# Kernel tuning notes

Measured on AMD Instinct MI355X. Metric: run time of the kernel, lower is better.

Reference implementation:

```python
import jax, jax.numpy as jnp
import numpy as np

B_, T_, D_ = 4, 4096, 512
H_, DH_ = 8, 64
N_HASHES, BUCKET = 4, 64
SELF_ATTN_VAL = -5e4  # TOKEN_SELF_ATTN_VALUE from reformer-pytorch


def setup_inputs() -> dict:
    key = jax.random.key(0)
    ks = jax.random.split(key, 12)
    s = 0.02
    return {
        "src": jax.random.normal(ks[0], (B_, T_, D_), jnp.float32),
        "Wqk": jax.random.normal(ks[1], (D_, D_), jnp.float32) * s,
        "Wv": jax.random.normal(ks[2], (D_, D_), jnp.float32) * s,
        "Wout": jax.random.normal(ks[3], (D_, D_), jnp.float32) * s,
        "bout": jnp.zeros((D_,), jnp.float32),
        "W1": jax.random.normal(ks[4], (D_, 2048), jnp.float32) * s,
        "b1": jnp.zeros((2048,), jnp.float32),
        "W2": jax.random.normal(ks[5], (2048, D_), jnp.float32) * s,
        "b2": jnp.zeros((D_,), jnp.float32),
        "gamma": jnp.ones((D_,), jnp.float32),
        "beta": jnp.zeros((D_,), jnp.float32),
        "rotations": jax.random.normal(ks[6], (DH_, N_HASHES, (T_ // BUCKET) // 2), jnp.float32),
    }


def _look_one_back(x):
    # concat each chunk with the previous chunk (wraparound), along the slot axis
    prev = jnp.concatenate([x[:, -1:], x[:, :-1]], axis=1)
    return jnp.concatenate([x, prev], axis=2)


def lsh_attention(qk, v, rotations):
    # qk, v: (B, T, d) with B = batch*heads; shared-QK LSH attention (non-causal,
    # attend_across_buckets=True, allow_duplicate_attention=True, no dropout)
    B, T, d = qk.shape
    n_buckets = T // BUCKET
    # --- hashing ---
    rv = jnp.einsum("btf,fhi->bhti", qk, rotations)          # (B, n_hashes, T, nb/2)
    rv = jnp.concatenate([rv, -rv], axis=-1)                  # (B, n_hashes, T, nb)
    buckets = jnp.argmax(rv, axis=-1)                         # (B, n_hashes, T)
    offsets = (jnp.arange(N_HASHES) * n_buckets)[None, :, None]
    buckets = (buckets + offsets).reshape(B, N_HASHES * T)
    # --- sort by (bucket, position) ---
    ticker = jnp.arange(N_HASHES * T)
    buckets_and_t = buckets * T + (ticker % T)[None, :]
    sticker = jnp.argsort(buckets_and_t, axis=-1)             # (B, n_hashes*T)
    undo_sort = jnp.argsort(sticker, axis=-1)
    st = sticker % T
    sqk = jnp.take_along_axis(qk, st[..., None], axis=1)      # (B, n_hashes*T, d)
    sv = jnp.take_along_axis(v, st[..., None], axis=1)
    # --- chunk ---
    chunks = N_HASHES * n_buckets
    bq_t = st.reshape(B, chunks, BUCKET)
    bqk = sqk.reshape(B, chunks, BUCKET, d)
    bv = sv.reshape(B, chunks, BUCKET, d)
    bq = bqk
    bk = bqk / (jnp.linalg.norm(bqk, axis=-1, keepdims=True) + 1e-6)
    bk = _look_one_back(bk)                                   # (B, chunks, 2*BUCKET, d)
    bv = _look_one_back(bv)
    bkv_t = _look_one_back(bq_t)                              # (B, chunks, 2*BUCKET)
    # --- attention within chunk (+ one look-back chunk) ---
    dots = jnp.einsum("bcie,bcje->bcij", bq, bk) * (d ** -0.5)
    self_mask = bq_t[:, :, :, None] == bkv_t[:, :, None, :]
    dots = jnp.where(self_mask, SELF_ATTN_VAL, dots)
    lse = jax.nn.logsumexp(dots, axis=-1, keepdims=True)
    p = jnp.exp(dots - lse)
    bo = jnp.einsum("bcij,bcje->bcie", p, bv)
    # --- unsort and combine hash rounds ---
    so = bo.reshape(B, N_HASHES * T, d)
    slog = lse.reshape(B, N_HASHES * T)
    o = jnp.take_along_axis(so, undo_sort[..., None], axis=1)
    logits = jnp.take_along_axis(slog, undo_sort, axis=1)
    o = o.reshape(B, N_HASHES, T, d)
    logits = logits.reshape(B, N_HASHES, T, 1)
    probs = jnp.exp(logits - jax.nn.logsumexp(logits, axis=1, keepdims=True))
    return jnp.sum(o * probs, axis=1)                         # (B, T, d)


def _layer(src, Wqk, Wv, Wout, bout, W1, b1, W2, b2, gamma, beta, rotations):
    b, t, dm = src.shape
    qk = src @ Wqk
    v = src @ Wv
    def split(x):
        return x.reshape(b, t, H_, DH_).transpose(0, 2, 1, 3).reshape(b * H_, t, DH_)
    o = lsh_attention(split(qk), split(v), rotations)
    o = o.reshape(b, H_, t, DH_).transpose(0, 2, 1, 3).reshape(b, t, dm)
    attn_out = o @ Wout + bout
    x = src + attn_out                # residual (dropout = identity in eval)
    ffn = jax.nn.relu(x @ W1 + b1) @ W2 + b2
    y = x + ffn
    mu = jnp.mean(y, axis=-1, keepdims=True)
    var = jnp.mean((y - mu) ** 2, axis=-1, keepdims=True)
    return (y - mu) / jnp.sqrt(var + 1e-6) * gamma + beta     # post-norm (norm2)


def reference(src, Wqk, Wv, Wout, bout, W1, b1, W2, b2, gamma, beta, rotations):
    return _layer(src, Wqk, Wv, Wout, bout, W1, b1, W2, b2, gamma, beta, rotations)
```

## Files before the change

kernel.cpp:

```cpp
#include <hip/hip_runtime.h>

#define B_ 4
#define T_ 4096
#define D_ 512
#define H_ 8
#define DH_ 64
#define NH_ 4
#define NB_ 64
#define BH_ (B_*H_)
#define CHUNKS_ (NH_*NB_)
#define NTICK_ (NH_*T_)
#define M_ (B_*T_)
#define FFN_ 2048

typedef __attribute__((ext_vector_type(8))) short bf16x8;
typedef __attribute__((ext_vector_type(4))) float f32x4;

__device__ __forceinline__ unsigned short f2bf(float x) {
  unsigned int u = __float_as_uint(x);
  return (unsigned short)((u + 0x7FFFu + ((u >> 16) & 1u)) >> 16);
}
__device__ __forceinline__ float bf2f(unsigned short s) {
  return __uint_as_float(((unsigned int)s) << 16);
}
__device__ __forceinline__ unsigned int cvt_pk_bf16(float lo, float hi) {
  unsigned int r;
  asm("v_cvt_pk_bf16_f32 %0, %1, %2" : "=v"(r) : "v"(lo), "v"(hi));
  return r;
}

__device__ __forceinline__ void gld_lds16(const void* g, void* l) {
  __builtin_amdgcn_global_load_lds(
      (const __attribute__((address_space(1))) unsigned int*)g,
      (__attribute__((address_space(3))) unsigned int*)l, 16, 0, 0);
}

__device__ __forceinline__ int swf(int row) { return (row ^ (row >> 3)) & 7; }
__device__ __forceinline__ int off64(int row, int k) {
  return row * 64 + (((k >> 3) ^ swf(row)) << 3) + (k & 7);
}
__device__ __forceinline__ int off128(int row, int k) {
  return row * 128 + (((k >> 3) ^ swf(row)) << 3) + (k & 7);
}

template<int OM>
__global__ __launch_bounds__(512) void gemm256(
    const unsigned short* __restrict__ A, const unsigned short* __restrict__ BT,
    const float* __restrict__ bias, unsigned short* __restrict__ Cb,
    unsigned short* __restrict__ Cb2, float* __restrict__ Cf,
    float* __restrict__ invn, int M, int N, int K)
{
  constexpr int ABSZ = 32768;
  __shared__ __align__(16) unsigned short smem[2 * ABSZ];
  const int tid = threadIdx.x;
  const int lane = tid & 63, w = tid >> 6;
  const int wm = (w >> 2) * 128, wn = (w & 3) * 64;
  const int g = lane >> 4, cl = lane & 15;

  const int gx = gridDim.x;
  const int id = blockIdx.x + blockIdx.y * gx;
  const int cpx = (gx * gridDim.y) >> 3;
  const int swz = (id & 7) * cpx + (id >> 3);
  const int m0 = (swz / gx) * 256, n0 = (swz % gx) * 256;

  const bool isv = (OM == 1) && (n0 >= 512);

  f32x4 acc[8][4];
#pragma unroll
  for (int i = 0; i < 8; ++i)
#pragma unroll
    for (int j = 0; j < 4; ++j) acc[i][j] = (f32x4){0.f, 0.f, 0.f, 0.f};

#define STG256(BUF, KB, P)                                                    \
  do {                                                                        \
    const bool isA_ = (P) < 2;                                                \
    const int half_ = (P) & 1;                                                \
    const unsigned short* Mp_ = isA_ ? A : BT;                                \
    const int gb_ = isA_ ? m0 : n0;                                           \
    const int ro_ = isA_ ? 0 : 16384;                                         \
    _Pragma("unroll")                                                         \
    for (int c2 = 0; c2 < 2; ++c2) {                                          \
      const int r_ = half_ * 128 + w * 16 + c2 * 8 + (lane >> 3);             \
      const int kg_ = (lane & 7) ^ swf(r_);                                   \
      gld_lds16(&Mp_[(size_t)(gb_ + r_) * K + (KB) + kg_ * 8],                \
                &smem[(BUF) * ABSZ + ro_ +                                    \
                      (half_ * 128 + w * 16 + c2 * 8) * 64 + lane * 8]);      \
    }                                                                         \
  } while (0)

#pragma unroll
  for (int p = 0; p < 4; ++p) STG256(0, 0, p);

  const int KT = K >> 6;
  for (int kt = 0; kt < KT; ++kt) {
    const int cur = kt & 1;
    const unsigned short* As = smem + cur * ABSZ;
    const unsigned short* Bs = As + 16384;
#pragma unroll
    for (int p = 0; p < 4; ++p) {
      if (kt + 1 < KT) STG256(cur ^ 1, (kt + 1) * 64, p);
      if (p == 0) {
        if (kt + 1 < KT) asm volatile("s_waitcnt vmcnt(2)" ::: "memory");
        else             asm volatile("s_waitcnt vmcnt(0)" ::: "memory");
        __builtin_amdgcn_s_barrier();
      }
      const int rq = wm + (p >> 1) * 64, cq = wn + (p & 1) * 32;
      bf16x8 af[4][2], bfr[2][2];
#pragma unroll
      for (int i = 0; i < 4; ++i)
#pragma unroll
        for (int kk = 0; kk < 2; ++kk)
          af[i][kk] = *(const bf16x8*)&As[off64(rq + i * 16 + cl, kk * 32 + g * 8)];
#pragma unroll
      for (int j = 0; j < 2; ++j)
#pragma unroll
        for (int kk = 0; kk < 2; ++kk)
          bfr[j][kk] = *(const bf16x8*)&Bs[off64(cq + j * 16 + cl, kk * 32 + g * 8)];
      __builtin_amdgcn_s_setprio(1);
#pragma unroll
      for (int kk = 0; kk < 2; ++kk)
#pragma unroll
        for (int i = 0; i < 4; ++i)
#pragma unroll
          for (int j = 0; j < 2; ++j)
            acc[(p >> 1) * 4 + i][(p & 1) * 2 + j] =
                __builtin_amdgcn_mfma_f32_16x16x32_bf16(
                    af[i][kk], bfr[j][kk], acc[(p >> 1) * 4 + i][(p & 1) * 2 + j], 0, 0, 0);
      __builtin_amdgcn_s_setprio(0);
      if (p == 3) __builtin_amdgcn_s_barrier();
    }
  }
#undef STG256

  float bv[4];
  if constexpr (OM == 0) {
#pragma unroll
    for (int j4 = 0; j4 < 4; ++j4) bv[j4] = bias[n0 + wn + j4 * 16 + cl];
  }
#pragma unroll
  for (int i = 0; i < 8; ++i) {
#pragma unroll
    for (int r = 0; r < 4; ++r) {
      const int lrow = wm + i * 16 + g * 4 + r;
      const int sw = (lrow & 7) << 3;
      float v4[4];
      float ss = 0.f;
#pragma unroll
      for (int j4 = 0; j4 < 4; ++j4) {
        float val = acc[i][j4][r];
        if constexpr (OM == 0) val = fmaxf(val + bv[j4], 0.f);
        v4[j4] = val;
        if constexpr (OM == 1) {
          if (!isv) {
            ss += val * val;
            Cf[(size_t)(m0 + lrow) * 512 + n0 + wn + j4 * 16 + cl] = val;
          }
        }
      }
#pragma unroll
      for (int j4 = 0; j4 < 4; j4 += 2) {
        const unsigned int pk = cvt_pk_bf16(v4[j4], v4[j4 + 1]);
        smem[lrow * 256 + ((wn + j4 * 16 + cl) ^ sw)]       = (unsigned short)pk;
        smem[lrow * 256 + ((wn + (j4 + 1) * 16 + cl) ^ sw)] = (unsigned short)(pk >> 16);
      }
      if constexpr (OM == 1) {
        if (!isv) {
          ss += __shfl_xor(ss, 1); ss += __shfl_xor(ss, 2);
          ss += __shfl_xor(ss, 4); ss += __shfl_xor(ss, 8);
          if (cl == 0) {
            const int m = m0 + lrow;
            const int bb = m >> 12, t = m & (T_ - 1);
            const int hh = ((n0 + wn) >> 6) & 7;
            invn[((size_t)(bb * 8 + hh)) * T_ + t] = 1.0f / (sqrtf(ss) + 1e-6f);
          }
        }
      }
    }
  }
  __syncthreads();
#pragma unroll
  for (int l = 0; l < 16; ++l) {
    const int idx = tid + l * 512;
    const int row = idx >> 5, c8 = (idx & 31) * 8;
    const uint4 u = *(const uint4*)&smem[row * 256 + (c8 ^ ((row & 7) << 3))];
    if constexpr (OM == 1) {
      if (isv)
        *(uint4*)&Cb2[(size_t)(m0 + row) * 512 + (n0 - 512) + c8] = u;
      else
        *(uint4*)&Cb[(size_t)(m0 + row) * 512 + n0 + c8] = u;
    } else {
      *(uint4*)&Cb[(size_t)(m0 + row) * N + n0 + c8] = u;
    }
  }
}

template<int BM, int MODE, bool HAS_BIAS, bool RELU, bool HAS_RESID>
__global__ __launch_bounds__(256) void gemm_bf16(
    const unsigned short* __restrict__ A, const unsigned short* __restrict__ BT,
    const float* __restrict__ bias, const unsigned short* __restrict__ resid,
    float* __restrict__ Cf, unsigned short* __restrict__ Cb,
    unsigned short* __restrict__ Cb2, float* __restrict__ invn,
    int M, int N, int K, int lda, int ldbt, int ldr)
{
  constexpr int MI = BM / 32;
  constexpr int ABSZ = (BM + 128) * 64;
  __shared__ __align__(16) unsigned short smem[2 * ABSZ];
  const int tid = threadIdx.x;
  const int lane = tid & 63;
  const int w = tid >> 6;
  const int wm = (w >> 1) * (BM / 2), wn = (w & 1) * 64;
  const int g = lane >> 4, cl = lane & 15;

  const int gx = gridDim.x;
  const int id = blockIdx.x + blockIdx.y * gx;
  const int cpx = (gx * gridDim.y) >> 3;
  const int swz = (id & 7) * cpx + (id >> 3);
  const int m0 = (swz / gx) * BM, n0 = (swz % gx) * 128;

  f32x4 acc[MI][4];
#pragma unroll
  for (int i = 0; i < MI; ++i)
#pragma unroll
    for (int j = 0; j < 4; ++j) acc[i][j] = (f32x4){0.f, 0.f, 0.f, 0.f};

  const int srow = tid >> 3;
  const int skc  = (tid & 7) * 8;

#define STAGE(BUF, K0)                                                        \
  do {                                                                        \
    unsigned short* As_ = smem + (BUF) * ABSZ;                                \
    unsigned short* Bs_ = As_ + BM * 64;                                      \
    _Pragma("unroll")                                                         \
    for (int ci = 0; ci < BM / 32; ++ci)                                      \
      gld_lds16(&A[(size_t)(m0 + ci * 32 + srow) * lda + (K0) + skc],         \
                &As_[ci * 2048 + tid * 8]);                                   \
    _Pragma("unroll")                                                         \
    for (int ci = 0; ci < 4; ++ci)                                            \
      gld_lds16(&BT[(size_t)(n0 + ci * 32 + srow) * ldbt + (K0) + skc],       \
                &Bs_[ci * 2048 + tid * 8]);                                   \
  } while (0)

  STAGE(0, 0);
  const int KT = K >> 6;
  for (int kt = 0; kt < KT; ++kt) {
    if (kt + 1 < KT) {
      STAGE((kt + 1) & 1, (kt + 1) * 64);
      asm volatile("s_waitcnt vmcnt(8)" ::: "memory");
    } else {
      asm volatile("s_waitcnt vmcnt(0)" ::: "memory");
    }
    __builtin_amdgcn_s_barrier();
    const unsigned short* As = smem + (kt & 1) * ABSZ;
    const unsigned short* Bs = As + BM * 64;
#pragma unroll
    for (int kk = 0; kk < 64; kk += 32) {
      bf16x8 af[MI], bfr[4];
#pragma unroll
      for (int i = 0; i < MI; ++i)
        af[i] = *(const bf16x8*)&As[(wm + i * 16 + cl) * 64 + kk + g * 8];
#pragma unroll
      for (int j = 0; j < 4; ++j)
        bfr[j] = *(const bf16x8*)&Bs[(wn + j * 16 + cl) * 64 + kk + g * 8];
#pragma unroll
      for (int i = 0; i < MI; ++i)
#pragma unroll
        for (int j = 0; j < 4; ++j)
          acc[i][j] = __builtin_amdgcn_mfma_f32_16x16x32_bf16(af[i], bfr[j], acc[i][j], 0, 0, 0);
    }
    asm volatile("" ::: "memory");
    __builtin_amdgcn_s_barrier();
  }
#undef STAGE

  float bv[4];
  if constexpr (HAS_BIAS) {
#pragma unroll
    for (int j = 0; j < 4; ++j) bv[j] = bias[n0 + wn + j * 16 + cl];
  }
#pragma unroll
  for (int i = 0; i < MI; ++i) {
#pragma unroll
    for (int r = 0; r < 4; ++r) {
      const int lrow = wm + i * 16 + g * 4 + r;
      float v4[4];
#pragma unroll
      for (int j = 0; j < 4; ++j) {
        float val = acc[i][j][r];
        if constexpr (HAS_BIAS) val += bv[j];
        if constexpr (RELU) val = fmaxf(val, 0.f);
        v4[j] = val;
      }
      const unsigned int p01 = cvt_pk_bf16(v4[0], v4[1]);
      const unsigned int p23 = cvt_pk_bf16(v4[2], v4[3]);
      const int sw = (lrow & 7) << 3;
      smem[lrow * 128 + ((wn +  0 + cl) ^ sw)] = (unsigned short)p01;
      smem[lrow * 128 + ((wn + 16 + cl) ^ sw)] = (unsigned short)(p01 >> 16);
      smem[lrow * 128 + ((wn + 32 + cl) ^ sw)] = (unsigned short)p23;
      smem[lrow * 128 + ((wn + 48 + cl) ^ sw)] = (unsigned short)(p23 >> 16);
    }
  }
  __syncthreads();
#pragma unroll
  for (int l = 0; l < BM / 16; ++l) {
    const int idx = tid + l * 256;
    const int row = idx >> 4, c8 = (idx & 15) * 8;
    uint4 u = *(const uint4*)&smem[row * 128 + (c8 ^ ((row & 7) << 3))];
    if constexpr (HAS_RESID) {
      const uint4 rv = *(const uint4*)&resid[(size_t)(m0 + row) * ldr + n0 + c8];
      const unsigned short* sp = (const unsigned short*)&u;
      const unsigned short* rp = (const unsigned short*)&rv;
      float f[8];
#pragma unroll
      for (int e = 0; e < 8; ++e) f[e] = bf2f(sp[e]) + bf2f(rp[e]);
      u.x = cvt_pk_bf16(f[0], f[1]); u.y = cvt_pk_bf16(f[2], f[3]);
      u.z = cvt_pk_bf16(f[4], f[5]); u.w = cvt_pk_bf16(f[6], f[7]);
    }
    *(uint4*)&Cb[(size_t)(m0 + row) * N + n0 + c8] = u;
  }
}

__global__ __launch_bounds__(256) void prep_all(
    const float* __restrict__ Wqk, const float* __restrict__ Wv,
    const float* __restrict__ Wout, const float* __restrict__ W1,
    const float* __restrict__ W2, const float* __restrict__ src,
    unsigned short* __restrict__ WqkvT, unsigned short* __restrict__ WoutT,
    unsigned short* __restrict__ W1T, unsigned short* __restrict__ W2T,
    unsigned short* __restrict__ src_b)
{
  __shared__ float tile[32][33];
  int bid = blockIdx.x;
  if (bid >= 2816) {
    const int i = (bid - 2816) * 256 + threadIdx.x;
    const int m = i >> 6, d0 = (i & 63) * 8;
    float x[8];
    *(float4*)&x[0] = *(const float4*)&src[(size_t)m * D_ + d0];
    *(float4*)&x[4] = *(const float4*)&src[(size_t)m * D_ + d0 + 4];
    unsigned short hi[8];
#pragma unroll
    for (int e = 0; e < 8; ++e) hi[e] = f2bf(x[e]);
    *(uint4*)&src_b[(size_t)m * D_ + d0] = *(const uint4*)&hi[0];
    return;
  }
  const float* W; unsigned short* WT; int K, N, bx, by;
  if (bid < 256)        { W = Wqk;  WT = WqkvT; K = 512;  N = 512;
                          bx = bid & 15; by = bid >> 4; }
  else if (bid < 512)   { bid -= 256;  W = Wv; WT = WqkvT + (size_t)512 * 512;
                          K = 512; N = 512;
                          bx = bid & 15; by = bid >> 4; }
  else if (bid < 768)   { bid -= 512;  W = Wout; WT = WoutT; K = 512;  N = 512;
                          bx = bid & 15; by = bid >> 4; }
  else if (bid < 1792)  { bid -= 768;  W = W1;   WT = W1T;   K = 512;  N = 2048;
                          bx = bid & 63; by = bid >> 6; }
  else                  { bid -= 1792; W = W2;   WT = W2T;   K = 2048; N = 512;
                          bx = bid & 15; by = bid >> 4; }
  const int k0 = by * 32, n0 = bx * 32;
  const int tx = threadIdx.x & 31, ty = threadIdx.x >> 5;
#pragma unroll
  for (int r = 0; r < 32; r += 8)
    tile[ty + r][tx] = W[(size_t)(k0 + ty + r) * N + n0 + tx];
  __syncthreads();
#pragma unroll
  for (int r = 0; r < 32; r += 8)
    WT[(size_t)(n0 + ty + r) * K + k0 + tx] = f2bf(tile[tx][ty + r]);
}

__global__ __launch_bounds__(256) void hash_gemm_kernel(
    const float* __restrict__ qk, const float* __restrict__ rot,
    int* __restrict__ buckets)
{
  __shared__ __align__(16) float As[64][136];
  __shared__ __align__(16) float Bs[64][132];
  const int tid = threadIdx.x;
  const int tx = tid & 15, ty = tid >> 4;
  const int t0 = blockIdx.x * 128, bh = blockIdx.y;
  const int b = bh >> 3, hd = bh & 7;

#pragma unroll
  for (int l = 0; l < 8; ++l) {
    const int idx = tid + l * 256;
    const int row = idx >> 4;
    const int kq = (idx & 15) << 2;
    const float4 a = *(const float4*)&qk[((size_t)b * T_ + t0 + row) * D_ + hd * DH_ + kq];
    As[kq + 0][row] = a.x; As[kq + 1][row] = a.y;
    As[kq + 2][row] = a.z; As[kq + 3][row] = a.w;
  }
#pragma unroll
  for (int l = 0; l < 8; ++l) {
    const int idx = tid + l * 256;
    const int kr = idx >> 5;
    const int c4 = (idx & 31) << 2;
    *(float4*)&Bs[kr][c4] = *(const float4*)&rot[kr * 128 + c4];
  }
  __syncthreads();

  float acc[8][8];
#pragma unroll
  for (int i = 0; i < 8; ++i)
#pragma unroll
    for (int j = 0; j < 8; ++j) acc[i][j] = 0.f;

#pragma unroll 4
  for (int kk = 0; kk < 64; ++kk) {
    float a[8], bq[8];
    *(float4*)&a[0]  = *(const float4*)&As[kk][ty * 8];
    *(float4*)&a[4]  = *(const float4*)&As[kk][ty * 8 + 4];
    *(float4*)&bq[0] = *(const float4*)&Bs[kk][tx * 8];
    *(float4*)&bq[4] = *(const float4*)&Bs[kk][tx * 8 + 4];
#pragma unroll
    for (int i = 0; i < 8; ++i)
#pragma unroll
      for (int j = 0; j < 8; ++j)
        acc[i][j] = fmaf(a[i], bq[j], acc[i][j]);
  }
  __syncthreads();

  float* pval = &As[0][0];
  int*   pidx = (int*)&Bs[0][0];
  const int i0 = (tx & 3) * 8;
#pragma unroll
  for (int r = 0; r < 8; ++r) {
    float v = -3.0e38f; int idx = 127;
#pragma unroll
    for (int j = 0; j < 8; ++j) {
      const float p = acc[r][j];
      const int li = i0 + j;
      if (p > v || (p == v && li < idx)) { v = p; idx = li; }
      const float n = -p;
      const int ni = 32 + li;
      if (n > v || (n == v && ni < idx)) { v = n; idx = ni; }
    }
    pval[(ty * 8 + r) * 16 + tx] = v;
    pidx[(ty * 8 + r) * 16 + tx] = idx;
  }
  __syncthreads();

#pragma unroll
  for (int l = 0; l < 2; ++l) {
    const int id = tid + l * 256;
    const int tok = id >> 2, hh = id & 3;
    float v = pval[tok * 16 + hh * 4];
    int idx = pidx[tok * 16 + hh * 4];
#pragma unroll
    for (int e = 1; e < 4; ++e) {
      const float ov = pval[tok * 16 + hh * 4 + e];
      const int oi = pidx[tok * 16 + hh * 4 + e];
      if (ov > v || (ov == v && oi < idx)) { v = ov; idx = oi; }
    }
    buckets[((size_t)bh * NH_ + hh) * T_ + t0 + tok] = idx + hh * NB_;
  }
}

__global__ __launch_bounds__(256) void hist_kernel(
    const int* __restrict__ buckets, int* __restrict__ bstart)
{
  __shared__ int bins[256];
  const int bh = blockIdx.x;
  bins[threadIdx.x] = 0;
  __syncthreads();
  for (int e = threadIdx.x; e < NTICK_; e += 256)
    atomicAdd(&bins[buckets[(size_t)bh * NTICK_ + e]], 1);
  __syncthreads();
  if (threadIdx.x == 0) {
    int run = 0;
    for (int i = 0; i < 256; ++i) { const int c = bins[i]; bins[i] = run; run += c; }
  }
  __syncthreads();
  bstart[bh * 256 + threadIdx.x] = bins[threadIdx.x];
}

__global__ __launch_bounds__(64) void compact_kernel(
    const int* __restrict__ buckets, const int* __restrict__ bstart,
    int* __restrict__ sticker)
{
  const int bucket = blockIdx.x, bh = blockIdx.y;
  const int h = bucket >> 6;
  const int lane = threadIdx.x;
  int base = bstart[bh * 256 + bucket];
  const int* bk = buckets + (size_t)bh * NTICK_ + (size_t)h * T_;
  for (int it = 0; it < 64; ++it) {
    const int t = it * 64 + lane;
    const bool m = (bk[t] == bucket);
    const unsigned long long bal = __ballot(m);
    if (m) {
      const int pos = base + __popcll(bal & ((1ull << lane) - 1ull));
      sticker[(size_t)bh * NTICK_ + pos] = h * T_ + t;
    }
    base += __popcll(bal);
  }
}

__global__ __launch_bounds__(256) void attn_kernel(
    const unsigned short* __restrict__ qkb, const unsigned short* __restrict__ vb,
    const int* __restrict__ sticker, const float* __restrict__ invn,
    unsigned short* __restrict__ orowsb, float* __restrict__ logits)
{
  __shared__ __align__(16) unsigned short Rs[128 * 64];
  __shared__ __align__(16) unsigned short Vs[128 * 64];
  __shared__ int tks[128];
  __shared__ float invs[128];

  const int cx = blockIdx.x;
  const int c = (cx & 7) * 32 + (cx >> 3);
  const int bh = blockIdx.y;
  const int b = bh >> 3, hd = bh & 7;
  const int tid = threadIdx.x;
  const int hr = c >> 6;
  const int w = tid >> 6, lane = tid & 63, g = lane >> 4, cl = lane & 15;

  if (tid < 128) {
    const int sc = (tid < 64) ? c : ((c + CHUNKS_ - 1) & (CHUNKS_ - 1));
    const int tick = sticker[(size_t)bh * NTICK_ + sc * 64 + (tid & 63)];
    const int t = tick & (T_ - 1);
    tks[tid] = t;
    invs[tid] = invn[bh * T_ + t];
  }
  __syncthreads();

  {
    const int sr = lane >> 3, gq = lane & 7;
#pragma unroll
    for (int l = 0; l < 4; ++l) {
      const int row = l * 32 + w * 8 + sr;
      const size_t gb = ((size_t)b * T_ + tks[row]) * D_ + hd * DH_
                      + ((gq ^ swf(row)) << 3);
      const int dst = (l * 32 + w * 8) * 64 + lane * 8;
      gld_lds16(&qkb[gb], &Rs[dst]);
      gld_lds16(&vb[gb],  &Vs[dst]);
    }
  }
  __syncthreads();

  f32x4 sacc[8];
#pragma unroll
  for (int j = 0; j < 8; ++j) sacc[j] = (f32x4){0.f, 0.f, 0.f, 0.f};
  __builtin_amdgcn_s_setprio(1);
#pragma unroll
  for (int kk = 0; kk < 2; ++kk) {
    const bf16x8 aq = *(const bf16x8*)&Rs[off64(w * 16 + cl, kk * 32 + g * 8)];
#pragma unroll
    for (int j = 0; j < 8; ++j) {
      const bf16x8 bk = *(const bf16x8*)&Rs[off64(j * 16 + cl, kk * 32 + g * 8)];
      sacc[j] = __builtin_amdgcn_mfma_f32_16x16x32_bf16(aq, bk, sacc[j], 0, 0, 0);
    }
  }
  __builtin_amdgcn_s_setprio(0);
  const int d0 = (tid & 15) * 4, tg = tid >> 4;
  unsigned int qw[8][2];
#pragma unroll
  for (int e = 0; e < 8; ++e) {
    const uint2 q = *(const uint2*)&Vs[off64(tg * 8 + e, d0)];
    qw[e][0] = q.x; qw[e][1] = q.y;
  }
  __syncthreads();

  {
    unsigned short col[4][8];
#pragma unroll
    for (int e = 0; e < 8; ++e) {
      col[0][e] = (unsigned short)(qw[e][0] & 0xffffu);
      col[1][e] = (unsigned short)(qw[e][0] >> 16);
      col[2][e] = (unsigned short)(qw[e][1] & 0xffffu);
      col[3][e] = (unsigned short)(qw[e][1] >> 16);
    }
#pragma unroll
    for (int dd = 0; dd < 4; ++dd)
      *(uint4*)&Vs[off128(d0 + dd, tg * 8)] = *(const uint4*)&col[dd][0];
  }

  float iv[8]; int tk[8];
#pragma unroll
  for (int j = 0; j < 8; ++j) {
    iv[j] = invs[j * 16 + cl] * 0.125f;
    tk[j] = tks[j * 16 + cl];
  }
  float pinv[4];
#pragma unroll
  for (int r = 0; r < 4; ++r) {
    const int row = w * 16 + g * 4 + r;
    const int tq = tks[row];
    float e8[8];
    float sum = 0.f;
#pragma unroll
    for (int j = 0; j < 8; ++j) {
      float e = __expf(sacc[j][r] * iv[j]);
      if (tq == tk[j]) e = 0.f;
      e8[j] = e;
      sum += e;
    }
    sum += __shfl_xor(sum, 1); sum += __shfl_xor(sum, 2);
    sum += __shfl_xor(sum, 4); sum += __shfl_xor(sum, 8);
    pinv[r] = 1.f / sum;
#pragma unroll
    for (int j = 0; j < 8; j += 2) {
      const unsigned int pk = cvt_pk_bf16(e8[j], e8[j + 1]);
      Rs[off128(row, j * 16 + cl)]       = (unsigned short)pk;
      Rs[off128(row, (j + 1) * 16 + cl)] = (unsigned short)(pk >> 16);
    }
    if (cl == 0)
      logits[((size_t)bh * T_ + tq) * NH_ + hr] = __logf(sum);
  }
  __syncthreads();

  f32x4 oacc[4];
#pragma unroll
  for (int jd = 0; jd < 4; ++jd) oacc[jd] = (f32x4){0.f, 0.f, 0.f, 0.f};
  __builtin_amdgcn_s_setprio(1);
#pragma unroll
  for (int ks = 0; ks < 4; ++ks) {
    const bf16x8 pa = *(const bf16x8*)&Rs[off128(w * 16 + cl, ks * 32 + g * 8)];
#pragma unroll
    for (int jd = 0; jd < 4; ++jd) {
      const bf16x8 vv = *(const bf16x8*)&Vs[off128(jd * 16 + cl, ks * 32 + g * 8)];
      oacc[jd] = __builtin_amdgcn_mfma_f32_16x16x32_bf16(pa, vv, oacc[jd], 0, 0, 0);
    }
  }
  __builtin_amdgcn_s_setprio(0);
  __syncthreads();

#pragma unroll
  for (int r = 0; r < 4; ++r) {
    const int row = w * 16 + g * 4 + r;
    const unsigned int q01 = cvt_pk_bf16(oacc[0][r] * pinv[r], oacc[1][r] * pinv[r]);
    const unsigned int q23 = cvt_pk_bf16(oacc[2][r] * pinv[r], oacc[3][r] * pinv[r]);
    Rs[off64(row,      cl)] = (unsigned short)q01;
    Rs[off64(row, 16 + cl)] = (unsigned short)(q01 >> 16);
    Rs[off64(row, 32 + cl)] = (unsigned short)q23;
    Rs[off64(row, 48 + cl)] = (unsigned short)(q23 >> 16);
  }
  __syncthreads();

#pragma unroll
  for (int l = 0; l < 2; ++l) {
    const int idx = tid + l * 256;
    const int row = idx >> 3, k0 = (idx & 7) * 8;
    *(uint4*)&orowsb[(((size_t)bh * T_ + tks[row]) * NH_ + hr) * DH_ + k0] =
        *(const uint4*)&Rs[off64(row, k0)];
  }
}

__global__ __launch_bounds__(256) void combine_kernel(
    const unsigned short* __restrict__ orowsb, const float* __restrict__ logits,
    unsigned short* __restrict__ ocombb)
{
  const int gid = blockIdx.x * 4 + (threadIdx.x >> 6);
  const int lane = threadIdx.x & 63;
  const int bh = gid >> 12, t = gid & (T_ - 1);
  const int b = bh >> 3, hd = bh & 7;
  const float4 lg = *(const float4*)&logits[((size_t)bh * T_ + t) * NH_];
  const float m = fmaxf(fmaxf(lg.x, lg.y), fmaxf(lg.z, lg.w));
  const float w0 = __expf(lg.x - m), w1 = __expf(lg.y - m);
  const float w2 = __expf(lg.z - m), w3 = __expf(lg.w - m);
  const float inv = 1.f / (w0 + w1 + w2 + w3);
  const size_t rb = ((size_t)bh * T_ + t) * (NH_ * DH_) + lane;
  const float o = w0 * bf2f(orowsb[rb])
                + w1 * bf2f(orowsb[rb + DH_])
                + w2 * bf2f(orowsb[rb + 2 * DH_])
                + w3 * bf2f(orowsb[rb + 3 * DH_]);
  ocombb[((size_t)b * T_ + t) * D_ + hd * DH_ + lane] = f2bf(o * inv);
}

__global__ __launch_bounds__(256) void ln_kernel(
    const unsigned short* __restrict__ yb, const float* __restrict__ gamma,
    const float* __restrict__ beta, float* __restrict__ out)
{
  const int row = blockIdx.x * 4 + (threadIdx.x >> 6);
  const int lane = threadIdx.x & 63;
  const size_t base = (size_t)row * D_ + lane * 8;
  const uint4 u = *(const uint4*)&yb[base];
  const unsigned short* up = (const unsigned short*)&u;
  float x[8];
#pragma unroll
  for (int i = 0; i < 8; ++i) x[i] = bf2f(up[i]);
  float s = 0.f;
#pragma unroll
  for (int i = 0; i < 8; ++i) s += x[i];
#pragma unroll
  for (int m = 32; m >= 1; m >>= 1) s += __shfl_xor(s, m);
  const float mu = s * (1.f / D_);
  float vs = 0.f;
#pragma unroll
  for (int i = 0; i < 8; ++i) { const float d = x[i] - mu; vs += d * d; }
#pragma unroll
  for (int m = 32; m >= 1; m >>= 1) vs += __shfl_xor(vs, m);
  const float rstd = rsqrtf(vs * (1.f / D_) + 1e-6f);
  float gm[8], bt[8];
  *(float4*)&gm[0] = *(const float4*)&gamma[lane * 8];
  *(float4*)&gm[4] = *(const float4*)&gamma[lane * 8 + 4];
  *(float4*)&bt[0] = *(const float4*)&beta[lane * 8];
  *(float4*)&bt[4] = *(const float4*)&beta[lane * 8 + 4];
  float o[8];
#pragma unroll
  for (int i = 0; i < 8; ++i) o[i] = (x[i] - mu) * rstd * gm[i] + bt[i];
  *(float4*)&out[base]     = make_float4(o[0], o[1], o[2], o[3]);
  *(float4*)&out[base + 4] = make_float4(o[4], o[5], o[6], o[7]);
}

extern "C" void kernel_launch(void* const* d_in, const int* in_sizes, int n_in,
                              void* d_out, int out_size, void* d_ws, size_t ws_size,
                              hipStream_t stream) {
  (void)in_sizes; (void)n_in; (void)out_size; (void)ws_size;
  const float* src   = (const float*)d_in[0];
  const float* Wqk   = (const float*)d_in[1];
  const float* Wv    = (const float*)d_in[2];
  const float* Wout  = (const float*)d_in[3];
  const float* bout  = (const float*)d_in[4];
  const float* W1    = (const float*)d_in[5];
  const float* b1    = (const float*)d_in[6];
  const float* W2    = (const float*)d_in[7];
  const float* b2    = (const float*)d_in[8];
  const float* gamma = (const float*)d_in[9];
  const float* beta  = (const float*)d_in[10];
  const float* rot   = (const float*)d_in[11];
  float* out = (float*)d_out;

  char* ws = (char*)d_ws;
  const size_t MB = 1024 * 1024;
  float*          qk      = (float*)(ws);
  unsigned short* src_b   = (unsigned short*)(ws + 32 * MB);
  unsigned short* v_b     = (unsigned short*)(ws + 48 * MB);
  unsigned short* orows_b = (unsigned short*)(ws + 64 * MB);
  unsigned short* qk_b    = (unsigned short*)(ws + 128 * MB);
  char* p = ws + 144 * MB;
  float* logits  = (float*)p; p += (size_t)BH_ * T_ * NH_ * 4;
  int*   buckets = (int*)p;   p += (size_t)BH_ * NH_ * T_ * 4;
  int*   sticker = (int*)p;   p += (size_t)BH_ * NTICK_ * 4;
  int*   bstart  = (int*)p;   p += (size_t)BH_ * 256 * 4;
  float* invn    = (float*)p; p += (size_t)BH_ * T_ * 4;
  unsigned short* WqkvT = (unsigned short*)p; p += (size_t)1024 * 512 * 2;
  unsigned short* WoutT = (unsigned short*)p; p += (size_t)D_ * D_ * 2;
  unsigned short* W1T   = (unsigned short*)p; p += (size_t)FFN_ * D_ * 2;
  unsigned short* W2T   = (unsigned short*)p; p += (size_t)D_ * FFN_ * 2;

  unsigned short* ocomb_b  = qk_b;
  unsigned short* x_b      = v_b;
  unsigned short* hidden_b = orows_b;
  unsigned short* ybuf_b   = (unsigned short*)ws;

  prep_all<<<2816 + M_ * D_ / 8 / 256, 256, 0, stream>>>(
      Wqk, Wv, Wout, W1, W2, src, WqkvT, WoutT, W1T, W2T, src_b);

  gemm256<1><<<dim3(1024 / 256, M_ / 256), 512, 0, stream>>>(
      src_b, WqkvT, nullptr, qk_b, v_b, qk, invn, M_, 1024, D_);
  hash_gemm_kernel<<<dim3(T_ / 128, BH_), 256, 0, stream>>>(qk, rot, buckets);
  hist_kernel<<<BH_, 256, 0, stream>>>(buckets, bstart);
  compact_kernel<<<dim3(256, BH_), 64, 0, stream>>>(buckets, bstart, sticker);
  attn_kernel<<<dim3(CHUNKS_, BH_), 256, 0, stream>>>(
      qk_b, v_b, sticker, invn, orows_b, logits);
  combine_kernel<<<BH_ * T_ / 4, 256, 0, stream>>>(orows_b, logits, ocomb_b);
  gemm_bf16<128, 1, true, false, true>
      <<<dim3(D_ / 128, M_ / 128), 256, 0, stream>>>(
      ocomb_b, WoutT, bout, src_b, nullptr, x_b, nullptr, nullptr,
      M_, D_, D_, D_, D_, D_);
  gemm256<0><<<dim3(FFN_ / 256, M_ / 256), 512, 0, stream>>>(
      x_b, W1T, b1, hidden_b, nullptr, nullptr, nullptr, M_, FFN_, D_);
  gemm_bf16<128, 1, true, false, true>
      <<<dim3(D_ / 128, M_ / 128), 256, 0, stream>>>(
      hidden_b, W2T, b2, x_b, nullptr, ybuf_b, nullptr, nullptr,
      M_, D_, FFN_, FFN_, FFN_, D_);
  ln_kernel<<<M_ / 4, 256, 0, stream>>>(ybuf_b, gamma, beta, out);
}
```

Before: 321.3 us.

## Replace N=512 GEMMs with 256x128 tile, 512-thread swizzled pipelined kernel

The generic 128x128 bf16 GEMM used for the output projection and the FFN down-projection is replaced by a 256x128 tile kernel with 8 waves. It uses XOR-swizzled LDS staging (reusing the swz/off64 helpers from gemm256), interleaves next-tile global-to-LDS loads with the MFMA phases, and raises wave priority around the MFMA bursts. The aim is more reuse of each loaded B tile, fewer LDS bank conflicts and better overlap of loads with compute. The cost is that the grid for N=512 halves to 256 blocks, which could underfill the GPU's compute units.

```diff
diff --git a/kernel.cpp b/kernel.cpp
--- a/kernel.cpp
+++ b/kernel.cpp
@@ -194,115 +194,108 @@
   }
 }
 
-template<int BM, int MODE, bool HAS_BIAS, bool RELU, bool HAS_RESID>
-__global__ __launch_bounds__(256) void gemm_bf16(
+template<bool HAS_RESID>
+__global__ __launch_bounds__(512) void gemm256x128(
     const unsigned short* __restrict__ A, const unsigned short* __restrict__ BT,
     const float* __restrict__ bias, const unsigned short* __restrict__ resid,
-    float* __restrict__ Cf, unsigned short* __restrict__ Cb,
-    unsigned short* __restrict__ Cb2, float* __restrict__ invn,
-    int M, int N, int K, int lda, int ldbt, int ldr)
-{
-  constexpr int MI = BM / 32;
-  constexpr int ABSZ = (BM + 128) * 64;
+    unsigned short* __restrict__ Cb, int M, int N, int K, int ldr)
+{
+  constexpr int ABSZ = 24576;
   __shared__ __align__(16) unsigned short smem[2 * ABSZ];
   const int tid = threadIdx.x;
-  const int lane = tid & 63;
-  const int w = tid >> 6;
-  const int wm = (w >> 1) * (BM / 2), wn = (w & 1) * 64;
+  const int lane = tid & 63, w = tid >> 6;
+  const int wm = (w >> 2) * 128, wn = (w & 3) * 32;
   const int g = lane >> 4, cl = lane & 15;
 
   const int gx = gridDim.x;
   const int id = blockIdx.x + blockIdx.y * gx;
   const int cpx = (gx * gridDim.y) >> 3;
   const int swz = (id & 7) * cpx + (id >> 3);
-  const int m0 = (swz / gx) * BM, n0 = (swz % gx) * 128;
-
-  f32x4 acc[MI][4];
-#pragma unroll
-  for (int i = 0; i < MI; ++i)
-#pragma unroll
-    for (int j = 0; j < 4; ++j) acc[i][j] = (f32x4){0.f, 0.f, 0.f, 0.f};
-
-  const int srow = tid >> 3;
-  const int skc  = (tid & 7) * 8;
-
-#define STAGE(BUF, K0)                                                        \
+  const int m0 = (swz / gx) * 256, n0 = (swz % gx) * 128;
+
+  f32x4 acc[8][2];
+#pragma unroll
+  for (int i = 0; i < 8; ++i)
+#pragma unroll
+    for (int j = 0; j < 2; ++j) acc[i][j] = (f32x4){0.f, 0.f, 0.f, 0.f};
+
+#define STG128(BUF, KB, P)                                                    \
   do {                                                                        \
-    unsigned short* As_ = smem + (BUF) * ABSZ;                                \
-    unsigned short* Bs_ = As_ + BM * 64;                                      \
-    _Pragma("unroll")                                                         \
-    for (int ci = 0; ci < BM / 32; ++ci)                                      \
-      gld_lds16(&A[(size_t)(m0 + ci * 32 + srow) * lda + (K0) + skc],         \
-                &As_[ci * 2048 + tid * 8]);                                   \
-    _Pragma("unroll")                                                         \
-    for (int ci = 0; ci < 4; ++ci)                                            \
-      gld_lds16(&BT[(size_t)(n0 + ci * 32 + srow) * ldbt + (K0) + skc],       \
-                &Bs_[ci * 2048 + tid * 8]);                                   \
+    if ((P) < 3) {                                                            \
+      const bool isA_ = (P) < 2;                                              \
+      const int half_ = (P) & 1;                                              \
+      const unsigned short* Mp_ = isA_ ? A : BT;                              \
+      const int gb_ = isA_ ? m0 : n0;                                         \
+      const int ro_ = isA_ ? half_ * 8192 : 16384;                            \
+      _Pragma("unroll")                                                       \
+      for (int c2 = 0; c2 < 2; ++c2) {                                        \
+        const int rr_ = w * 16 + c2 * 8 + (lane >> 3);                        \
+        const int r_ = (isA_ ? half_ * 128 : 0) + rr_;                        \
+        const int kg_ = (lane & 7) ^ swf(r_);                                 \
+        gld_lds16(&Mp_[(size_t)(gb_ + r_) * K + (KB) + kg_ * 8],              \
+                  &smem[(BUF) * ABSZ + ro_ + rr_ * 64 + lane * 8]);           \
+      }                                                                       \
+    }                                                                         \
   } while (0)
 
-  STAGE(0, 0);
+#pragma unroll
+  for (int p = 0; p < 3; ++p) STG128(0, 0, p);
+
   const int KT = K >> 6;
   for (int kt = 0; kt < KT; ++kt) {
-    if (kt + 1 < KT) {
-      STAGE((kt + 1) & 1, (kt + 1) * 64);
-      asm volatile("s_waitcnt vmcnt(8)" ::: "memory");
-    } else {
-      asm volatile("s_waitcnt vmcnt(0)" ::: "memory");
-    }
-    __builtin_amdgcn_s_barrier();
-    const unsigned short* As = smem + (kt & 1) * ABSZ;
-    const unsigned short* Bs = As + BM * 64;
-#pragma unroll
-    for (int kk = 0; kk < 64; kk += 32) {
-      bf16x8 af[MI], bfr[4];
-#pragma unroll
-      for (int i = 0; i < MI; ++i)
-        af[i] = *(const bf16x8*)&As[(wm + i * 16 + cl) * 64 + kk + g * 8];
-#pragma unroll
-      for (int j = 0; j < 4; ++j)
-        bfr[j] = *(const bf16x8*)&Bs[(wn + j * 16 + cl) * 64 + kk + g * 8];
-#pragma unroll
-      for (int i = 0; i < MI; ++i)
-#pragma unroll
-        for (int j = 0; j < 4; ++j)
-          acc[i][j] = __builtin_amdgcn_mfma_f32_16x16x32_bf16(af[i], bfr[j], acc[i][j], 0, 0, 0);
-    }
-    asm volatile("" ::: "memory");
-    __builtin_amdgcn_s_barrier();
-  }
-#undef STAGE
-
-  float bv[4];
-  if constexpr (HAS_BIAS) {
-#pragma unroll
-    for (int j = 0; j < 4; ++j) bv[j] = bias[n0 + wn + j * 16 + cl];
-  }
-#pragma unroll
-  for (int i = 0; i < MI; ++i) {
+    const int cur = kt & 1;
+    const unsigned short* As = smem + cur * ABSZ;
+    const unsigned short* Bs = As + 16384;
+#pragma unroll
+    for (int p = 0; p < 4; ++p) {
+      if (kt + 1 < KT) STG128(cur ^ 1, (kt + 1) * 64, p);
+      if (p == 0) {
+        if (kt + 1 < KT) asm volatile("s_waitcnt vmcnt(2)" ::: "memory");
+        else             asm volatile("s_waitcnt vmcnt(0)" ::: "memory");
+        __builtin_amdgcn_s_barrier();
+      }
+      const int rq = wm + (p >> 1) * 64, cq = wn + (p & 1) * 16;
+      bf16x8 af[4][2], bfr[2];
+#pragma unroll
+      for (int i = 0; i < 4; ++i)
+#pragma unroll
+        for (int kk = 0; kk < 2; ++kk)
+          af[i][kk] = *(const bf16x8*)&As[off64(rq + i * 16 + cl, kk * 32 + g * 8)];
+#pragma unroll
+      for (int kk = 0; kk < 2; ++kk)
+        bfr[kk] = *(const bf16x8*)&Bs[off64(cq + cl, kk * 32 + g * 8)];
+      __builtin_amdgcn_s_setprio(1);
+#pragma unroll
+      for (int kk = 0; kk < 2; ++kk)
+#pragma unroll
+        for (int i = 0; i < 4; ++i)
+          acc[(p >> 1) * 4 + i][p & 1] =
+              __builtin_amdgcn_mfma_f32_16x16x32_bf16(
+                  af[i][kk], bfr[kk], acc[(p >> 1) * 4 + i][p & 1], 0, 0, 0);
+      __builtin_amdgcn_s_setprio(0);
+      if (p == 3) __builtin_amdgcn_s_barrier();
+    }
+  }
+#undef STG128
+
+  float bv[2];
+#pragma unroll
+  for (int j = 0; j < 2; ++j) bv[j] = bias[n0 + wn + j * 16 + cl];
+#pragma unroll
+  for (int i = 0; i < 8; ++i) {
 #pragma unroll
     for (int r = 0; r < 4; ++r) {
       const int lrow = wm + i * 16 + g * 4 + r;
-      float v4[4];
-#pragma unroll
-      for (int j = 0; j < 4; ++j) {
-        float val = acc[i][j][r];
-        if constexpr (HAS_BIAS) val += bv[j];
-        if constexpr (RELU) val = fmaxf(val, 0.f);
-        v4[j] = val;
-      }
-      const unsigned int p01 = cvt_pk_bf16(v4[0], v4[1]);
-      const unsigned int p23 = cvt_pk_bf16(v4[2], v4[3]);
       const int sw = (lrow & 7) << 3;
-      smem[lrow * 128 + ((wn +  0 + cl) ^ sw)] = (unsigned short)p01;
-      smem[lrow * 128 + ((wn + 16 + cl) ^ sw)] = (unsigned short)(p01 >> 16);
-      smem[lrow * 128 + ((wn + 32 + cl) ^ sw)] = (unsigned short)p23;
-      smem[lrow * 128 + ((wn + 48 + cl) ^ sw)] = (unsigned short)(p23 >> 16);
-    }
-  }
-  __syncthreads();
-#pragma unroll
-  for (int l = 0; l < BM / 16; ++l) {
-    const int idx = tid + l * 256;
+      const unsigned int pk = cvt_pk_bf16(acc[i][0][r] + bv[0], acc[i][1][r] + bv[1]);
+      smem[lrow * 128 + ((wn + cl) ^ sw)]      = (unsigned short)pk;
+      smem[lrow * 128 + ((wn + 16 + cl) ^ sw)] = (unsigned short)(pk >> 16);
+    }
+  }
+  __syncthreads();
+#pragma unroll
+  for (int l = 0; l < 8; ++l) {
+    const int idx = tid + l * 512;
     const int row = idx >> 4, c8 = (idx & 15) * 8;
     uint4 u = *(const uint4*)&smem[row * 128 + (c8 ^ ((row & 7) << 3))];
     if constexpr (HAS_RESID) {
@@ -747,15 +740,11 @@
   attn_kernel<<<dim3(CHUNKS_, BH_), 256, 0, stream>>>(
       qk_b, v_b, sticker, invn, orows_b, logits);
   combine_kernel<<<BH_ * T_ / 4, 256, 0, stream>>>(orows_b, logits, ocomb_b);
-  gemm_bf16<128, 1, true, false, true>
-      <<<dim3(D_ / 128, M_ / 128), 256, 0, stream>>>(
-      ocomb_b, WoutT, bout, src_b, nullptr, x_b, nullptr, nullptr,
-      M_, D_, D_, D_, D_, D_);
+  gemm256x128<true><<<dim3(D_ / 128, M_ / 256), 512, 0, stream>>>(
+      ocomb_b, WoutT, bout, src_b, x_b, M_, D_, D_, D_);
   gemm256<0><<<dim3(FFN_ / 256, M_ / 256), 512, 0, stream>>>(
       x_b, W1T, b1, hidden_b, nullptr, nullptr, nullptr, M_, FFN_, D_);
-  gemm_bf16<128, 1, true, false, true>
-      <<<dim3(D_ / 128, M_ / 128), 256, 0, stream>>>(
-      hidden_b, W2T, b2, x_b, nullptr, ybuf_b, nullptr, nullptr,
-      M_, D_, FFN_, FFN_, FFN_, D_);
+  gemm256x128<true><<<dim3(D_ / 128, M_ / 256), 512, 0, stream>>>(
+      hidden_b, W2T, b2, x_b, ybuf_b, M_, D_, FFN_, D_);
   ln_kernel<<<M_ / 4, 256, 0, stream>>>(ybuf_b, gamma, beta, out);
 }
```

Measured after the change: 334.8 us. +4.2%, slower.
